# Kernel tuning notes

Hardware: AMD Instinct MI355X
Metric: run time of the kernel (lower is better)

The kernel has to match this reference:

```python
import jax, jax.numpy as jnp
import numpy as np

HIDDEN = 1024
N_HEADS = 16
HEAD = HIDDEN // N_HEADS  # 64
DFF = 4 * HIDDEN


def setup_inputs() -> dict:
    key = jax.random.key(0)
    ks = jax.random.split(key, 12)
    B, T = 4, 2048
    s = 0.02
    return {
        "x": jax.random.normal(ks[0], (B, T, HIDDEN), jnp.float32),
        # per-head QKV weights, stacked: [H, HIDDEN, HEAD] (no bias, as in Head)
        "Wq": jax.random.normal(ks[1], (N_HEADS, HIDDEN, HEAD), jnp.float32) * s,
        "Wk": jax.random.normal(ks[2], (N_HEADS, HIDDEN, HEAD), jnp.float32) * s,
        "Wv": jax.random.normal(ks[3], (N_HEADS, HIDDEN, HEAD), jnp.float32) * s,
        "Wo": jax.random.normal(ks[4], (HIDDEN, HIDDEN), jnp.float32) * s,
        "bo": jnp.zeros((HIDDEN,), jnp.float32),
        "W1": jax.random.normal(ks[5], (HIDDEN, DFF), jnp.float32) * s,
        "b1": jnp.zeros((DFF,), jnp.float32),
        "W2": jax.random.normal(ks[6], (DFF, HIDDEN), jnp.float32) * s,
        "b2": jnp.zeros((HIDDEN,), jnp.float32),
        "g1": jnp.ones((HIDDEN,), jnp.float32),
        "be1": jnp.zeros((HIDDEN,), jnp.float32),
        "g2": jnp.ones((HIDDEN,), jnp.float32),
        "be2": jnp.zeros((HIDDEN,), jnp.float32),
    }


def _layernorm(x, g, b, eps=1e-5):
    mu = jnp.mean(x, axis=-1, keepdims=True)
    var = jnp.mean(jnp.square(x - mu), axis=-1, keepdims=True)
    return (x - mu) * jax.lax.rsqrt(var + eps) * g + b


def _attention(h, Wq, Wk, Wv, Wo, bo):
    B, T, C = h.shape
    # [B,T,C] x [H,C,D] -> [B,H,T,D]
    Q = jnp.einsum('btc,hcd->bhtd', h, Wq)
    K = jnp.einsum('btc,hcd->bhtd', h, Wk)
    V = jnp.einsum('btc,hcd->bhtd', h, Wv)
    scores = jnp.einsum('bhtd,bhsd->bhts', Q, K) / np.sqrt(HEAD).astype(np.float32)
    causal = jnp.tril(jnp.ones((T, T), bool))
    scores = jnp.where(causal, scores, -jnp.inf)
    attn = jax.nn.softmax(scores, axis=-1)
    out = jnp.einsum('bhts,bhsd->bhtd', attn, V)
    # concat heads in order (head axis -> last dim blocks)
    out = out.transpose(0, 2, 1, 3).reshape(B, T, C)
    return out @ Wo + bo


def reference(x, Wq, Wk, Wv, Wo, bo, W1, b1, W2, b2, g1, be1, g2, be2):
    x = x + _attention(_layernorm(x, g1, be1), Wq, Wk, Wv, Wo, bo)
    h = _layernorm(x, g2, be2)
    ff = jax.nn.relu(h @ W1 + b1) @ W2 + b2
    return x + ff
```

## Files before the change

### kernel.cpp

```cpp
#include <hip/hip_runtime.h>
#include <hip/hip_bf16.h>
#include <stdint.h>


#define HID 1024
#define NH 16
#define HD 64
#define DFF 4096
#define BATCH 4
#define SEQ 2048
#define NTOK (BATCH*SEQ)

typedef unsigned short u16;
typedef __attribute__((ext_vector_type(4))) float f32x4;
typedef __attribute__((ext_vector_type(8))) __bf16 bf16x8;

__device__ __forceinline__ u16 f2bf(float f) {
    unsigned int u = __float_as_uint(f);
    u = (u + 0x7fffu + ((u >> 16) & 1u)) >> 16;
    return (u16)u;
}

__device__ __forceinline__ void gload_lds16(const void* g, void* lds) {
    __builtin_amdgcn_global_load_lds(
        (const __attribute__((address_space(1))) unsigned int*)(uintptr_t)g,
        (__attribute__((address_space(3))) unsigned int*)(uintptr_t)lds, 16, 0, 0);
}

__global__ __launch_bounds__(256) void ln_kernel(const float* __restrict__ x,
                                                 const float* __restrict__ g,
                                                 const float* __restrict__ be,
                                                 u16* __restrict__ out) {
    __shared__ float red[10];
    const int row = blockIdx.x, tid = threadIdx.x;
    const float4 v = ((const float4*)(x + (size_t)row * HID))[tid];
    float s  = v.x + v.y + v.z + v.w;
    float s2 = v.x*v.x + v.y*v.y + v.z*v.z + v.w*v.w;
    for (int off = 32; off > 0; off >>= 1) {
        s  += __shfl_down(s, off, 64);
        s2 += __shfl_down(s2, off, 64);
    }
    if ((tid & 63) == 0) { red[tid >> 6] = s; red[4 + (tid >> 6)] = s2; }
    __syncthreads();
    if (tid == 0) {
        red[8] = red[0] + red[1] + red[2] + red[3];
        red[9] = red[4] + red[5] + red[6] + red[7];
    }
    __syncthreads();
    const float mu  = red[8] * (1.f / HID);
    const float var = red[9] * (1.f / HID) - mu * mu;
    const float rstd = rsqrtf(var + 1e-5f);
    const float4 g4 = ((const float4*)g)[tid];
    const float4 b4 = ((const float4*)be)[tid];
    ushort4 o;
    o.x = f2bf((v.x - mu) * rstd * g4.x + b4.x);
    o.y = f2bf((v.y - mu) * rstd * g4.y + b4.y);
    o.z = f2bf((v.z - mu) * rstd * g4.z + b4.z);
    o.w = f2bf((v.w - mu) * rstd * g4.w + b4.w);
    ((ushort4*)(out + (size_t)row * HID))[tid] = o;
}

__global__ __launch_bounds__(256) void transpose_w(const float* __restrict__ in,
                                                   u16* __restrict__ out, int R, int C) {
    __shared__ float t[32][33];
    const int r0 = blockIdx.x * 32, c0 = blockIdx.y * 32;
    const float* inb = in + (size_t)blockIdx.z * R * C;
    u16* outb = out + (size_t)blockIdx.z * R * C;
    const int tid = threadIdx.x;
    const int tr = tid >> 3, tc = (tid & 7) * 4;
    const float4 v = *(const float4*)&inb[(size_t)(r0 + tr) * C + c0 + tc];
    t[tr][tc] = v.x; t[tr][tc + 1] = v.y; t[tr][tc + 2] = v.z; t[tr][tc + 3] = v.w;
    __syncthreads();
    ushort4 o;
    o.x = f2bf(t[tc + 0][tr]);
    o.y = f2bf(t[tc + 1][tr]);
    o.z = f2bf(t[tc + 2][tr]);
    o.w = f2bf(t[tc + 3][tr]);
    *(ushort4*)&outb[(size_t)(c0 + tr) * R + r0 + tc] = o;
}

__global__ __launch_bounds__(256) void transpose_v(const u16* __restrict__ in,
                                                   u16* __restrict__ out) {
    __shared__ u16 t[64][65];
    const int s0 = blockIdx.x * 64;
    const size_t bh = blockIdx.y;
    const u16* inb = in + bh * SEQ * HD;
    u16* outb = out + bh * HD * SEQ;
    const int tid = threadIdx.x;
    const int r = tid >> 2, c = (tid & 3) * 16;
    bf16x8 a = *(const bf16x8*)&inb[(size_t)(s0 + r) * HD + c];
    bf16x8 b = *(const bf16x8*)&inb[(size_t)(s0 + r) * HD + c + 8];
    #pragma unroll
    for (int i = 0; i < 8; i++) {
        t[r][c + i]     = ((const u16*)&a)[i];
        t[r][c + 8 + i] = ((const u16*)&b)[i];
    }
    __syncthreads();
    u16 o0[8], o1[8];
    #pragma unroll
    for (int i = 0; i < 8; i++) { o0[i] = t[c + i][r]; o1[i] = t[c + 8 + i][r]; }
    *(bf16x8*)&outb[(size_t)r * SEQ + s0 + c]     = *(const bf16x8*)o0;
    *(bf16x8*)&outb[(size_t)r * SEQ + s0 + c + 8] = *(const bf16x8*)o1;
}

template <int MODE>
__global__ __launch_bounds__(256) void gemm_kernel(const u16* __restrict__ A,
                                                   const u16* __restrict__ B,
                                                   float* __restrict__ outf,
                                                   u16* __restrict__ outh,
                                                   const float* __restrict__ bias,
                                                   const float* __restrict__ resid,
                                                   int K, int N, float scale) {
    __shared__ u16 Al[128][32];
    __shared__ u16 Bl[128][32];
    const int tid = threadIdx.x;
    const int w = tid >> 6, l = tid & 63;
    const int wr = w >> 1, wc = w & 1;
    const int m0 = blockIdx.x * 128, n0 = blockIdx.y * 128;

    f32x4 acc[4][4] = {};

    const u16* Ag = A + (size_t)(m0 + w * 32) * K;
    const u16* Bg = B + (size_t)(n0 + w * 32) * K;
    const int lr = l >> 2;
    const int lc = (l & 3) * 8;

    for (int k0 = 0; k0 < K; k0 += 32) {
        __syncthreads();
        #pragma unroll
        for (int it = 0; it < 2; it++) {
            gload_lds16(Ag + (size_t)(it * 16 + lr) * K + k0 + lc, &Al[w * 32 + it * 16][0]);
            gload_lds16(Bg + (size_t)(it * 16 + lr) * K + k0 + lc, &Bl[w * 32 + it * 16][0]);
        }
        __syncthreads();
        bf16x8 af[4], bf[4];
        #pragma unroll
        for (int i = 0; i < 4; i++)
            af[i] = *(const bf16x8*)&Al[wr * 64 + i * 16 + (l & 15)][(l >> 4) * 8];
        #pragma unroll
        for (int i = 0; i < 4; i++)
            bf[i] = *(const bf16x8*)&Bl[wc * 64 + i * 16 + (l & 15)][(l >> 4) * 8];
        #pragma unroll
        for (int mi = 0; mi < 4; mi++)
            #pragma unroll
            for (int nj = 0; nj < 4; nj++)
                acc[mi][nj] = __builtin_amdgcn_mfma_f32_16x16x32_bf16(af[mi], bf[nj], acc[mi][nj], 0, 0, 0);
    }

    const int r00 = m0 + wr * 64 + ((l >> 4) << 2);
    const int c00 = n0 + wc * 64 + (l & 15);
    if (MODE == 0) {
        #pragma unroll
        for (int nj = 0; nj < 4; nj++) {
            const int c = c00 + nj * 16;
            const int h = c >> 6, d = c & 63;
            #pragma unroll
            for (int mi = 0; mi < 4; mi++)
                #pragma unroll
                for (int j = 0; j < 4; j++) {
                    const int r = r00 + mi * 16 + j;
                    const int b = r >> 11, t = r & (SEQ - 1);
                    outh[((size_t)(b * NH + h) * SEQ + t) * HD + d] = f2bf(acc[mi][nj][j] * scale);
                }
        }
    } else if (MODE == 1) {
        #pragma unroll
        for (int nj = 0; nj < 4; nj++) {
            const int c = c00 + nj * 16;
            const float bi = bias[c];
            #pragma unroll
            for (int mi = 0; mi < 4; mi++)
                #pragma unroll
                for (int j = 0; j < 4; j++) {
                    const int r = r00 + mi * 16 + j;
                    const size_t idx = (size_t)r * N + c;
                    outf[idx] = resid[idx] + acc[mi][nj][j] + bi;
                }
        }
    } else {
        #pragma unroll
        for (int nj = 0; nj < 4; nj++) {
            const int c = c00 + nj * 16;
            const float bi = bias[c];
            #pragma unroll
            for (int mi = 0; mi < 4; mi++)
                #pragma unroll
                for (int j = 0; j < 4; j++) {
                    const int r = r00 + mi * 16 + j;
                    const float v = acc[mi][nj][j] + bi;
                    outh[(size_t)r * N + c] = f2bf(v > 0.f ? v : 0.f);
                }
        }
    }
}

__global__ __launch_bounds__(256) void attn_kernel(const u16* __restrict__ Q,
                                                   const u16* __restrict__ K,
                                                   const u16* __restrict__ Vt,
                                                   u16* __restrict__ O) {
    __shared__ u16 Kl[64 * 64];
    __shared__ u16 Vl[64 * 64];
    __shared__ u16 Pl[4][16 * 64];
    const int qt = blockIdx.x, bh = blockIdx.y;
    const int tid = threadIdx.x, w = tid >> 6, l = tid & 63;
    const int g = l >> 4, c16 = l & 15;

    const u16* Qg = Q + ((size_t)bh * SEQ + qt * 64 + w * 16) * HD;
    bf16x8 qf[2];
    qf[0] = *(const bf16x8*)&Qg[(size_t)c16 * HD + g * 8];
    qf[1] = *(const bf16x8*)&Qg[(size_t)c16 * HD + 32 + g * 8];

    f32x4 o[4] = {};
    float mrow[4], lrow[4];
    #pragma unroll
    for (int j = 0; j < 4; j++) { mrow[j] = -1e30f; lrow[j] = 0.f; }

    char* KlB = (char*)Kl;
    char* VlB = (char*)Vl;
    char* PlB = (char*)&Pl[w][0];

    for (int st = 0; st <= qt; ++st) {
        __syncthreads();
        {
            const u16* Kg = K + ((size_t)bh * SEQ + st * 64) * HD;
            const u16* Vg = Vt + (size_t)bh * HD * SEQ + st * 64;
            #pragma unroll
            for (int it = 0; it < 2; it++) {
                const int idx = it * 256 + tid;
                const int r = idx >> 3;
                const int cb = (idx & 7) * 16;
                bf16x8 kv = *(const bf16x8*)((const char*)Kg + (size_t)r * 128 + cb);
                *(bf16x8*)(KlB + r * 128 + (cb ^ ((r & 7) << 4))) = kv;
                bf16x8 vv = *(const bf16x8*)((const char*)Vg + (size_t)r * (SEQ * 2) + cb);
                *(bf16x8*)(VlB + r * 128 + (cb ^ ((r & 7) << 4))) = vv;
            }
        }
        __syncthreads();

        f32x4 s[4];
        #pragma unroll
        for (int n = 0; n < 4; n++) {
            const int row = n * 16 + c16;
            const char* base = KlB + row * 128;
            bf16x8 b0 = *(const bf16x8*)(base + ((g * 16) ^ ((row & 7) << 4)));
            bf16x8 b1 = *(const bf16x8*)(base + ((64 + g * 16) ^ ((row & 7) << 4)));
            f32x4 z = {};
            z = __builtin_amdgcn_mfma_f32_16x16x32_bf16(qf[0], b0, z, 0, 0, 0);
            s[n] = __builtin_amdgcn_mfma_f32_16x16x32_bf16(qf[1], b1, z, 0, 0, 0);
        }
        if (st == qt) {
            #pragma unroll
            for (int n = 0; n < 4; n++)
                #pragma unroll
                for (int j = 0; j < 4; j++) {
                    const int ql = w * 16 + g * 4 + j, sl = n * 16 + c16;
                    if (sl > ql) s[n][j] = -1e30f;
                }
        }
        #pragma unroll
        for (int j = 0; j < 4; j++) {
            float mx = fmaxf(fmaxf(s[0][j], s[1][j]), fmaxf(s[2][j], s[3][j]));
            for (int off = 1; off < 16; off <<= 1) mx = fmaxf(mx, __shfl_xor(mx, off, 64));
            const float newm = fmaxf(mrow[j], mx);
            const float sc = __expf(mrow[j] - newm);
            mrow[j] = newm;
            float ps = 0.f;
            #pragma unroll
            for (int n = 0; n < 4; n++) {
                const float p = __expf(s[n][j] - newm);
                s[n][j] = p; ps += p;
            }
            for (int off = 1; off < 16; off <<= 1) ps += __shfl_xor(ps, off, 64);
            lrow[j] = lrow[j] * sc + ps;
            #pragma unroll
            for (int n = 0; n < 4; n++) o[n][j] *= sc;
        }
        #pragma unroll
        for (int n = 0; n < 4; n++)
            #pragma unroll
            for (int j = 0; j < 4; j++) {
                const int row = g * 4 + j;
                const int cb = (n * 16 + c16) * 2;
                *(u16*)(PlB + row * 128 + (cb ^ ((row & 7) << 4))) = f2bf(s[n][j]);
            }
        bf16x8 pa[2];
        #pragma unroll
        for (int kb = 0; kb < 2; kb++) {
            const int row = c16;
            pa[kb] = *(const bf16x8*)(PlB + row * 128 + ((kb * 64 + g * 16) ^ ((row & 7) << 4)));
        }
        #pragma unroll
        for (int n = 0; n < 4; n++) {
            const int row = n * 16 + c16;
            const char* base = VlB + row * 128;
            bf16x8 v0 = *(const bf16x8*)(base + ((g * 16) ^ ((row & 7) << 4)));
            bf16x8 v1 = *(const bf16x8*)(base + ((64 + g * 16) ^ ((row & 7) << 4)));
            o[n] = __builtin_amdgcn_mfma_f32_16x16x32_bf16(pa[0], v0, o[n], 0, 0, 0);
            o[n] = __builtin_amdgcn_mfma_f32_16x16x32_bf16(pa[1], v1, o[n], 0, 0, 0);
        }
    }

    const int b = bh >> 4, h = bh & 15;
    #pragma unroll
    for (int j = 0; j < 4; j++) {
        const float inv = 1.f / lrow[j];
        const int t = qt * 64 + w * 16 + g * 4 + j;
        #pragma unroll
        for (int n = 0; n < 4; n++)
            O[((size_t)b * SEQ + t) * HID + h * HD + n * 16 + c16] = f2bf(o[n][j] * inv);
    }
}

extern "C" void kernel_launch(void* const* d_in, const int* in_sizes, int n_in,
                              void* d_out, int out_size, void* d_ws, size_t ws_size,
                              hipStream_t stream) {
    (void)in_sizes; (void)n_in; (void)out_size; (void)ws_size;
    const float* x   = (const float*)d_in[0];
    const float* Wq  = (const float*)d_in[1];
    const float* Wk  = (const float*)d_in[2];
    const float* Wv  = (const float*)d_in[3];
    const float* Wo  = (const float*)d_in[4];
    const float* bo  = (const float*)d_in[5];
    const float* W1  = (const float*)d_in[6];
    const float* b1  = (const float*)d_in[7];
    const float* W2  = (const float*)d_in[8];
    const float* b2  = (const float*)d_in[9];
    const float* g1  = (const float*)d_in[10];
    const float* be1 = (const float*)d_in[11];
    const float* g2  = (const float*)d_in[12];
    const float* be2 = (const float*)d_in[13];
    float* out = (float*)d_out;

    char* ws = (char*)d_ws;
    size_t off = 0;
    auto alloc = [&](size_t bytes) { void* p = ws + off; off += bytes; return p; };
    u16* Wq_t = (u16*)alloc((size_t)HID * HID * 2);
    u16* Wk_t = (u16*)alloc((size_t)HID * HID * 2);
    u16* Wv_t = (u16*)alloc((size_t)HID * HID * 2);
    u16* Wo_t = (u16*)alloc((size_t)HID * HID * 2);
    u16* W1_t = (u16*)alloc((size_t)DFF * HID * 2);
    u16* W2_t = (u16*)alloc((size_t)HID * DFF * 2);
    u16* h1   = (u16*)alloc((size_t)NTOK * HID * 2);
    u16* Qb   = (u16*)alloc((size_t)NTOK * HID * 2);
    u16* Kb   = (u16*)alloc((size_t)NTOK * HID * 2);
    u16* Vb   = (u16*)alloc((size_t)NTOK * HID * 2);
    u16* Vt   = (u16*)alloc((size_t)NTOK * HID * 2);
    float* x2 = (float*)alloc((size_t)NTOK * HID * 4);
    u16* ff1  = Qb;

    transpose_w<<<dim3(32, 2, 16), 256, 0, stream>>>(Wq, Wq_t, HID, HD);
    transpose_w<<<dim3(32, 2, 16), 256, 0, stream>>>(Wk, Wk_t, HID, HD);
    transpose_w<<<dim3(32, 2, 16), 256, 0, stream>>>(Wv, Wv_t, HID, HD);
    transpose_w<<<dim3(32, 32, 1), 256, 0, stream>>>(Wo, Wo_t, HID, HID);
    transpose_w<<<dim3(32, 128, 1), 256, 0, stream>>>(W1, W1_t, HID, DFF);
    transpose_w<<<dim3(128, 32, 1), 256, 0, stream>>>(W2, W2_t, DFF, HID);

    ln_kernel<<<NTOK, 256, 0, stream>>>(x, g1, be1, h1);

    gemm_kernel<0><<<dim3(64, 8), 256, 0, stream>>>(h1, Wq_t, nullptr, Qb, nullptr, nullptr, HID, HID, 0.125f);
    gemm_kernel<0><<<dim3(64, 8), 256, 0, stream>>>(h1, Wk_t, nullptr, Kb, nullptr, nullptr, HID, HID, 1.0f);
    gemm_kernel<0><<<dim3(64, 8), 256, 0, stream>>>(h1, Wv_t, nullptr, Vb, nullptr, nullptr, HID, HID, 1.0f);

    transpose_v<<<dim3(SEQ / 64, BATCH * NH), 256, 0, stream>>>(Vb, Vt);

    u16* attn_out = Vb;
    attn_kernel<<<dim3(SEQ / 64, BATCH * NH), 256, 0, stream>>>(Qb, Kb, Vt, attn_out);

    gemm_kernel<1><<<dim3(64, 8), 256, 0, stream>>>(attn_out, Wo_t, x2, nullptr, bo, x, HID, HID, 1.f);

    ln_kernel<<<NTOK, 256, 0, stream>>>(x2, g2, be2, h1);

    gemm_kernel<2><<<dim3(64, 32), 256, 0, stream>>>(h1, W1_t, nullptr, ff1, b1, nullptr, HID, DFF, 1.f);

    gemm_kernel<1><<<dim3(64, 8), 256, 0, stream>>>(ff1, W2_t, out, nullptr, b2, x2, DFF, HID, 1.f);
}
```

Before: 696.5 us.

## Fuse QKV GEMM and rewrite flash attention with 32x32 MFMA and prefetch

Concatenates the Q, K and V weight transposes into one buffer and runs a single fused QKV GEMM launch, with the output pointer and scale chosen per column block. The attention kernel is rewritten to use 128-query tiles with 32x32x16 MFMAs and double-buffered K/V LDS tiles filled through register prefetch. It keeps P in registers via cvt_pk and permlane32 swaps instead of staging through LDS, skips the rescale when the max grows by at most 8, and launches heaviest tiles first. This cuts launch count, LDS round trips and tail imbalance, at the cost of higher register pressure and more complex indexing. The fused QKV path relies on Qb, Kb and Vb being contiguous in the workspace.

Result: faster. 583.7 us (-16.2%).

```diff
diff --git a/kernel.cpp b/kernel.cpp
--- a/kernel.cpp
+++ b/kernel.cpp
@@ -12,13 +12,25 @@
 #define NTOK (BATCH*SEQ)
 
 typedef unsigned short u16;
+typedef unsigned int u32;
 typedef __attribute__((ext_vector_type(4))) float f32x4;
+typedef __attribute__((ext_vector_type(16))) float f32x16;
 typedef __attribute__((ext_vector_type(8))) __bf16 bf16x8;
 
 __device__ __forceinline__ u16 f2bf(float f) {
     unsigned int u = __float_as_uint(f);
     u = (u + 0x7fffu + ((u >> 16) & 1u)) >> 16;
     return (u16)u;
+}
+
+__device__ __forceinline__ u32 cvtpk(float lo, float hi) {
+    u32 d;
+    asm("v_cvt_pk_bf16_f32 %0, %1, %2" : "=v"(d) : "v"(lo), "v"(hi));
+    return d;
+}
+
+__device__ __forceinline__ void plswap(u32& a, u32& b) {
+    asm volatile("v_permlane32_swap_b32 %0, %1" : "+v"(a), "+v"(b));
 }
 
 __device__ __forceinline__ void gload_lds16(const void* g, void* lds) {
@@ -110,7 +122,7 @@
                                                    u16* __restrict__ outh,
                                                    const float* __restrict__ bias,
                                                    const float* __restrict__ resid,
-                                                   int K, int N, float scale) {
+                                                   int K, int N) {
     __shared__ u16 Al[128][32];
     __shared__ u16 Bl[128][32];
     const int tid = threadIdx.x;
@@ -133,18 +145,18 @@
             gload_lds16(Bg + (size_t)(it * 16 + lr) * K + k0 + lc, &Bl[w * 32 + it * 16][0]);
         }
         __syncthreads();
-        bf16x8 af[4], bf[4];
+        bf16x8 af[4], bfr[4];
         #pragma unroll
         for (int i = 0; i < 4; i++)
             af[i] = *(const bf16x8*)&Al[wr * 64 + i * 16 + (l & 15)][(l >> 4) * 8];
         #pragma unroll
         for (int i = 0; i < 4; i++)
-            bf[i] = *(const bf16x8*)&Bl[wc * 64 + i * 16 + (l & 15)][(l >> 4) * 8];
+            bfr[i] = *(const bf16x8*)&Bl[wc * 64 + i * 16 + (l & 15)][(l >> 4) * 8];
         #pragma unroll
         for (int mi = 0; mi < 4; mi++)
             #pragma unroll
             for (int nj = 0; nj < 4; nj++)
-                acc[mi][nj] = __builtin_amdgcn_mfma_f32_16x16x32_bf16(af[mi], bf[nj], acc[mi][nj], 0, 0, 0);
+                acc[mi][nj] = __builtin_amdgcn_mfma_f32_16x16x32_bf16(af[mi], bfr[nj], acc[mi][nj], 0, 0, 0);
     }
 
     const int r00 = m0 + wr * 64 + ((l >> 4) << 2);
@@ -153,14 +165,17 @@
         #pragma unroll
         for (int nj = 0; nj < 4; nj++) {
             const int c = c00 + nj * 16;
-            const int h = c >> 6, d = c & 63;
+            const int which = c >> 10, hc = c & 1023;
+            const int h = hc >> 6, d = hc & 63;
+            const float sc2 = (which == 0) ? 0.125f : 1.0f;
+            u16* outp = outh + (size_t)which * ((size_t)NTOK * HID);
             #pragma unroll
             for (int mi = 0; mi < 4; mi++)
                 #pragma unroll
                 for (int j = 0; j < 4; j++) {
                     const int r = r00 + mi * 16 + j;
                     const int b = r >> 11, t = r & (SEQ - 1);
-                    outh[((size_t)(b * NH + h) * SEQ + t) * HD + d] = f2bf(acc[mi][nj][j] * scale);
+                    outp[((size_t)(b * NH + h) * SEQ + t) * HD + d] = f2bf(acc[mi][nj][j] * sc2);
                 }
         }
     } else if (MODE == 1) {
@@ -198,117 +213,188 @@
                                                    const u16* __restrict__ K,
                                                    const u16* __restrict__ Vt,
                                                    u16* __restrict__ O) {
-    __shared__ u16 Kl[64 * 64];
-    __shared__ u16 Vl[64 * 64];
-    __shared__ u16 Pl[4][16 * 64];
-    const int qt = blockIdx.x, bh = blockIdx.y;
+    __shared__ u16 Kl[2][64 * 64];
+    __shared__ u16 Vl[2][64 * 64];
+    const int qt = (gridDim.x - 1) - blockIdx.x;
+    const int bh = blockIdx.y;
     const int tid = threadIdx.x, w = tid >> 6, l = tid & 63;
-    const int g = l >> 4, c16 = l & 15;
-
-    const u16* Qg = Q + ((size_t)bh * SEQ + qt * 64 + w * 16) * HD;
-    bf16x8 qf[2];
-    qf[0] = *(const bf16x8*)&Qg[(size_t)c16 * HD + g * 8];
-    qf[1] = *(const bf16x8*)&Qg[(size_t)c16 * HD + 32 + g * 8];
-
-    f32x4 o[4] = {};
-    float mrow[4], lrow[4];
+    const int q32 = l & 31, hi = l >> 5;
+    const int qbase = qt * 128 + w * 32;
+    const int qrow = qbase + q32;
+
+    const u16* Qg = Q + ((size_t)bh * SEQ + qrow) * HD;
+    bf16x8 qf[4];
     #pragma unroll
-    for (int j = 0; j < 4; j++) { mrow[j] = -1e30f; lrow[j] = 0.f; }
-
-    char* KlB = (char*)Kl;
-    char* VlB = (char*)Vl;
-    char* PlB = (char*)&Pl[w][0];
-
-    for (int st = 0; st <= qt; ++st) {
+    for (int c = 0; c < 4; ++c)
+        qf[c] = *(const bf16x8*)&Qg[c * 16 + hi * 8];
+
+    f32x16 oa[2] = {};
+    float m = -1e30f, lsum = 0.f;
+
+    const u16* Kg0 = K + (size_t)bh * SEQ * HD;
+    const u16* Vg0 = Vt + (size_t)bh * HD * SEQ;
+    const int sr = tid >> 2;
+    const int scb = (tid & 3) * 32;
+
+    bf16x8 kreg[2], vreg[2];
+    auto load_tile = [&](int st) {
+        const char* Kg = (const char*)(Kg0 + (size_t)st * 64 * HD);
+        const char* Vg = (const char*)(Vg0 + st * 64);
+        #pragma unroll
+        for (int it = 0; it < 2; it++) {
+            kreg[it] = *(const bf16x8*)(Kg + (size_t)sr * 128 + scb + it * 16);
+            vreg[it] = *(const bf16x8*)(Vg + (size_t)sr * (SEQ * 2) + scb + it * 16);
+        }
+    };
+    auto write_tile = [&](int buf) {
+        char* KlB = (char*)Kl[buf];
+        char* VlB = (char*)Vl[buf];
+        const int sw = (sr & 7) << 4;
+        #pragma unroll
+        for (int it = 0; it < 2; it++) {
+            *(bf16x8*)(KlB + sr * 128 + ((scb + it * 16) ^ sw)) = kreg[it];
+            *(bf16x8*)(VlB + sr * 128 + ((scb + it * 16) ^ sw)) = vreg[it];
+        }
+    };
+
+    const int ntiles = 2 * qt + 2;
+    const int tlast = (qbase + 31) >> 6;
+
+    load_tile(0);
+    write_tile(0);
+
+    for (int st = 0; st < ntiles; ++st) {
+        const int cur = st & 1;
         __syncthreads();
-        {
-            const u16* Kg = K + ((size_t)bh * SEQ + st * 64) * HD;
-            const u16* Vg = Vt + (size_t)bh * HD * SEQ + st * 64;
-            #pragma unroll
-            for (int it = 0; it < 2; it++) {
-                const int idx = it * 256 + tid;
-                const int r = idx >> 3;
-                const int cb = (idx & 7) * 16;
-                bf16x8 kv = *(const bf16x8*)((const char*)Kg + (size_t)r * 128 + cb);
-                *(bf16x8*)(KlB + r * 128 + (cb ^ ((r & 7) << 4))) = kv;
-                bf16x8 vv = *(const bf16x8*)((const char*)Vg + (size_t)r * (SEQ * 2) + cb);
-                *(bf16x8*)(VlB + r * 128 + (cb ^ ((r & 7) << 4))) = vv;
+        const bool pf = (st + 1 < ntiles);
+        if (pf) load_tile(st + 1);
+
+        if (st <= tlast) {
+            const char* KlB = (const char*)Kl[cur];
+            const char* VlB = (const char*)Vl[cur];
+
+            f32x16 s[2];
+            __builtin_amdgcn_s_setprio(1);
+            #pragma unroll
+            for (int a = 0; a < 2; ++a) {
+                const int row = a * 32 + q32;
+                const char* base = KlB + row * 128;
+                const int sw = (row & 7) << 4;
+                f32x16 accs = {};
+                #pragma unroll
+                for (int ds4 = 0; ds4 < 4; ++ds4) {
+                    bf16x8 kf = *(const bf16x8*)(base + ((ds4 * 32 + hi * 16) ^ sw));
+                    accs = __builtin_amdgcn_mfma_f32_32x32x16_bf16(kf, qf[ds4], accs, 0, 0, 0);
+                }
+                s[a] = accs;
             }
-        }
-        __syncthreads();
-
-        f32x4 s[4];
-        #pragma unroll
-        for (int n = 0; n < 4; n++) {
-            const int row = n * 16 + c16;
-            const char* base = KlB + row * 128;
-            bf16x8 b0 = *(const bf16x8*)(base + ((g * 16) ^ ((row & 7) << 4)));
-            bf16x8 b1 = *(const bf16x8*)(base + ((64 + g * 16) ^ ((row & 7) << 4)));
-            f32x4 z = {};
-            z = __builtin_amdgcn_mfma_f32_16x16x32_bf16(qf[0], b0, z, 0, 0, 0);
-            s[n] = __builtin_amdgcn_mfma_f32_16x16x32_bf16(qf[1], b1, z, 0, 0, 0);
-        }
-        if (st == qt) {
-            #pragma unroll
-            for (int n = 0; n < 4; n++)
-                #pragma unroll
-                for (int j = 0; j < 4; j++) {
-                    const int ql = w * 16 + g * 4 + j, sl = n * 16 + c16;
-                    if (sl > ql) s[n][j] = -1e30f;
-                }
-        }
-        #pragma unroll
-        for (int j = 0; j < 4; j++) {
-            float mx = fmaxf(fmaxf(s[0][j], s[1][j]), fmaxf(s[2][j], s[3][j]));
-            for (int off = 1; off < 16; off <<= 1) mx = fmaxf(mx, __shfl_xor(mx, off, 64));
-            const float newm = fmaxf(mrow[j], mx);
-            const float sc = __expf(mrow[j] - newm);
-            mrow[j] = newm;
-            float ps = 0.f;
-            #pragma unroll
-            for (int n = 0; n < 4; n++) {
-                const float p = __expf(s[n][j] - newm);
-                s[n][j] = p; ps += p;
+            __builtin_amdgcn_s_setprio(0);
+
+            if (st == tlast) {
+                const int st64 = st * 64;
+                #pragma unroll
+                for (int a = 0; a < 2; ++a)
+                    #pragma unroll
+                    for (int r = 0; r < 16; ++r) {
+                        const int kvg = st64 + a * 32 + (r & 3) + 8 * (r >> 2) + 4 * hi;
+                        if (kvg > qrow) s[a][r] = -1e30f;
+                    }
             }
-            for (int off = 1; off < 16; off <<= 1) ps += __shfl_xor(ps, off, 64);
-            lrow[j] = lrow[j] * sc + ps;
-            #pragma unroll
-            for (int n = 0; n < 4; n++) o[n][j] *= sc;
-        }
-        #pragma unroll
-        for (int n = 0; n < 4; n++)
-            #pragma unroll
-            for (int j = 0; j < 4; j++) {
-                const int row = g * 4 + j;
-                const int cb = (n * 16 + c16) * 2;
-                *(u16*)(PlB + row * 128 + (cb ^ ((row & 7) << 4))) = f2bf(s[n][j]);
+
+            float pm0 = -1e30f, pm1 = -1e30f, pm2 = -1e30f, pm3 = -1e30f;
+            #pragma unroll
+            for (int r = 0; r < 16; r += 4) {
+                pm0 = fmaxf(pm0, fmaxf(s[0][r + 0], s[1][r + 0]));
+                pm1 = fmaxf(pm1, fmaxf(s[0][r + 1], s[1][r + 1]));
+                pm2 = fmaxf(pm2, fmaxf(s[0][r + 2], s[1][r + 2]));
+                pm3 = fmaxf(pm3, fmaxf(s[0][r + 3], s[1][r + 3]));
             }
-        bf16x8 pa[2];
-        #pragma unroll
-        for (int kb = 0; kb < 2; kb++) {
-            const int row = c16;
-            pa[kb] = *(const bf16x8*)(PlB + row * 128 + ((kb * 64 + g * 16) ^ ((row & 7) << 4)));
-        }
-        #pragma unroll
-        for (int n = 0; n < 4; n++) {
-            const int row = n * 16 + c16;
-            const char* base = VlB + row * 128;
-            bf16x8 v0 = *(const bf16x8*)(base + ((g * 16) ^ ((row & 7) << 4)));
-            bf16x8 v1 = *(const bf16x8*)(base + ((64 + g * 16) ^ ((row & 7) << 4)));
-            o[n] = __builtin_amdgcn_mfma_f32_16x16x32_bf16(pa[0], v0, o[n], 0, 0, 0);
-            o[n] = __builtin_amdgcn_mfma_f32_16x16x32_bf16(pa[1], v1, o[n], 0, 0, 0);
-        }
+            float pmax = fmaxf(fmaxf(pm0, pm1), fmaxf(pm2, pm3));
+            pmax = fmaxf(pmax, __shfl_xor(pmax, 32, 64));
+
+            if (!__all(pmax <= m + 8.f)) {
+                const float newm = fmaxf(m, pmax);
+                const float sc = __expf(m - newm);
+                m = newm;
+                lsum *= sc;
+                #pragma unroll
+                for (int d = 0; d < 2; ++d)
+                    #pragma unroll
+                    for (int r = 0; r < 16; ++r)
+                        oa[d][r] *= sc;
+            }
+
+            float s0 = 0.f, s1 = 0.f, s2 = 0.f, s3 = 0.f;
+            #pragma unroll
+            for (int a = 0; a < 2; ++a)
+                #pragma unroll
+                for (int r = 0; r < 16; r += 4) {
+                    float p0 = __expf(s[a][r + 0] - m);
+                    float p1 = __expf(s[a][r + 1] - m);
+                    float p2 = __expf(s[a][r + 2] - m);
+                    float p3 = __expf(s[a][r + 3] - m);
+                    s[a][r + 0] = p0; s[a][r + 1] = p1;
+                    s[a][r + 2] = p2; s[a][r + 3] = p3;
+                    s0 += p0; s1 += p1; s2 += p2; s3 += p3;
+                }
+            float psum = (s0 + s1) + (s2 + s3);
+            psum += __shfl_xor(psum, 32, 64);
+            lsum += psum;
+
+            u32 W[2][4][2];
+            #pragma unroll
+            for (int a = 0; a < 2; ++a)
+                #pragma unroll
+                for (int i = 0; i < 4; ++i) {
+                    W[a][i][0] = cvtpk(s[a][4 * i + 0], s[a][4 * i + 1]);
+                    W[a][i][1] = cvtpk(s[a][4 * i + 2], s[a][4 * i + 3]);
+                }
+            bf16x8 pa[4];
+            #pragma unroll
+            for (int a = 0; a < 2; ++a)
+                #pragma unroll
+                for (int j = 0; j < 2; ++j) {
+                    u32 a0 = W[a][2 * j][0], b0 = W[a][2 * j + 1][0];
+                    u32 a1 = W[a][2 * j][1], b1 = W[a][2 * j + 1][1];
+                    plswap(a0, b0);
+                    plswap(a1, b1);
+                    union { u32 ww[4]; bf16x8 v; } u_;
+                    u_.ww[0] = a0; u_.ww[1] = a1; u_.ww[2] = b0; u_.ww[3] = b1;
+                    pa[2 * a + j] = u_.v;
+                }
+
+            __builtin_amdgcn_s_setprio(1);
+            #pragma unroll
+            for (int dblk = 0; dblk < 2; ++dblk) {
+                const int row = dblk * 32 + q32;
+                const char* base = VlB + row * 128;
+                const int sw = (row & 7) << 4;
+                #pragma unroll
+                for (int s4 = 0; s4 < 4; ++s4) {
+                    bf16x8 vf = *(const bf16x8*)(base + ((s4 * 32 + hi * 16) ^ sw));
+                    oa[dblk] = __builtin_amdgcn_mfma_f32_32x32x16_bf16(vf, pa[s4], oa[dblk], 0, 0, 0);
+                }
+            }
+            __builtin_amdgcn_s_setprio(0);
+        }
+
+        if (pf) write_tile(cur ^ 1);
     }
 
     const int b = bh >> 4, h = bh & 15;
+    const float inv = 1.f / lsum;
+    u16* Orow = O + ((size_t)b * SEQ + qrow) * HID + h * HD;
     #pragma unroll
-    for (int j = 0; j < 4; j++) {
-        const float inv = 1.f / lrow[j];
-        const int t = qt * 64 + w * 16 + g * 4 + j;
-        #pragma unroll
-        for (int n = 0; n < 4; n++)
-            O[((size_t)b * SEQ + t) * HID + h * HD + n * 16 + c16] = f2bf(o[n][j] * inv);
-    }
+    for (int dblk = 0; dblk < 2; ++dblk)
+        #pragma unroll
+        for (int i = 0; i < 4; ++i) {
+            ushort4 st4;
+            st4.x = f2bf(oa[dblk][4 * i + 0] * inv);
+            st4.y = f2bf(oa[dblk][4 * i + 1] * inv);
+            st4.z = f2bf(oa[dblk][4 * i + 2] * inv);
+            st4.w = f2bf(oa[dblk][4 * i + 3] * inv);
+            *(ushort4*)&Orow[dblk * 32 + 8 * i + 4 * hi] = st4;
+        }
 }
 
 extern "C" void kernel_launch(void* const* d_in, const int* in_sizes, int n_in,
@@ -334,9 +420,7 @@
     char* ws = (char*)d_ws;
     size_t off = 0;
     auto alloc = [&](size_t bytes) { void* p = ws + off; off += bytes; return p; };
-    u16* Wq_t = (u16*)alloc((size_t)HID * HID * 2);
-    u16* Wk_t = (u16*)alloc((size_t)HID * HID * 2);
-    u16* Wv_t = (u16*)alloc((size_t)HID * HID * 2);
+    u16* Wqkv_t = (u16*)alloc((size_t)3 * HID * HID * 2);
     u16* Wo_t = (u16*)alloc((size_t)HID * HID * 2);
     u16* W1_t = (u16*)alloc((size_t)DFF * HID * 2);
     u16* W2_t = (u16*)alloc((size_t)HID * DFF * 2);
@@ -348,29 +432,28 @@
     float* x2 = (float*)alloc((size_t)NTOK * HID * 4);
     u16* ff1  = Qb;
 
-    transpose_w<<<dim3(32, 2, 16), 256, 0, stream>>>(Wq, Wq_t, HID, HD);
-    transpose_w<<<dim3(32, 2, 16), 256, 0, stream>>>(Wk, Wk_t, HID, HD);
-    transpose_w<<<dim3(32, 2, 16), 256, 0, stream>>>(Wv, Wv_t, HID, HD);
+    transpose_w<<<dim3(32, 2, 16), 256, 0, stream>>>(Wq, Wqkv_t, HID, HD);
+    transpose_w<<<dim3(32, 2, 16), 256, 0, stream>>>(Wk, Wqkv_t + (size_t)HID * HID, HID, HD);
+    transpose_w<<<dim3(32, 2, 16), 256, 0, stream>>>(Wv, Wqkv_t + (size_t)2 * HID * HID, HID, HD);
     transpose_w<<<dim3(32, 32, 1), 256, 0, stream>>>(Wo, Wo_t, HID, HID);
     transpose_w<<<dim3(32, 128, 1), 256, 0, stream>>>(W1, W1_t, HID, DFF);
     transpose_w<<<dim3(128, 32, 1), 256, 0, stream>>>(W2, W2_t, DFF, HID);
 
     ln_kernel<<<NTOK, 256, 0, stream>>>(x, g1, be1, h1);
 
-    gemm_kernel<0><<<dim3(64, 8), 256, 0, stream>>>(h1, Wq_t, nullptr, Qb, nullptr, nullptr, HID, HID, 0.125f);
-    gemm_kernel<0><<<dim3(64, 8), 256, 0, stream>>>(h1, Wk_t, nullptr, Kb, nullptr, nullptr, HID, HID, 1.0f);
-    gemm_kernel<0><<<dim3(64, 8), 256, 0, stream>>>(h1, Wv_t, nullptr, Vb, nullptr, nullptr, HID, HID, 1.0f);
+    gemm_kernel<0><<<dim3(64, 24), 256, 0, stream>>>(h1, Wqkv_t, nullptr, Qb,
+                                                     nullptr, nullptr, HID, 3072);
 
     transpose_v<<<dim3(SEQ / 64, BATCH * NH), 256, 0, stream>>>(Vb, Vt);
 
     u16* attn_out = Vb;
-    attn_kernel<<<dim3(SEQ / 64, BATCH * NH), 256, 0, stream>>>(Qb, Kb, Vt, attn_out);
-
-    gemm_kernel<1><<<dim3(64, 8), 256, 0, stream>>>(attn_out, Wo_t, x2, nullptr, bo, x, HID, HID, 1.f);
+    attn_kernel<<<dim3(SEQ / 128, BATCH * NH), 256, 0, stream>>>(Qb, Kb, Vt, attn_out);
+
+    gemm_kernel<1><<<dim3(64, 8), 256, 0, stream>>>(attn_out, Wo_t, x2, nullptr, bo, x, HID, HID);
 
     ln_kernel<<<NTOK, 256, 0, stream>>>(x2, g2, be2, h1);
 
-    gemm_kernel<2><<<dim3(64, 32), 256, 0, stream>>>(h1, W1_t, nullptr, ff1, b1, nullptr, HID, DFF, 1.f);
-
-    gemm_kernel<1><<<dim3(64, 8), 256, 0, stream>>>(ff1, W2_t, out, nullptr, b2, x2, DFF, HID, 1.f);
-}
+    gemm_kernel<2><<<dim3(64, 32), 256, 0, stream>>>(h1, W1_t, nullptr, ff1, b1, nullptr, HID, DFF);
+
+    gemm_kernel<1><<<dim3(64, 8), 256, 0, stream>>>(ff1, W2_t, out, nullptr, b2, x2, DFF, HID);
+}
```
